# Kernel tuning notes

Measured on AMD Instinct MI355X. Metric: run time of the kernel, lower is better.

Reference implementation:

```python
import jax, jax.numpy as jnp
import numpy as np

N = 8192  # graph nodes (input_size)
B = 8     # batch size
MAX_DIFFUSION_STEP = 2
K_TOT = 2 * MAX_DIFFUSION_STEP + 1  # 2 kernels * 2 steps + identity term


def setup_inputs() -> dict:
    key = jax.random.key(0)
    k_in, k_h, k0, k1, k_w, k_b = jax.random.split(key, 6)
    scale = 0.5 / np.sqrt(N)  # keep spectral norm ~<1 so Chebyshev recursion is stable
    return {
        "input": jax.random.normal(k_in, (B, N), dtype=jnp.float32),
        "hidden": jax.random.normal(k_h, (B, N), dtype=jnp.float32),
        "kernel0": jax.random.normal(k0, (N, N), dtype=jnp.float32) * scale,
        "kernel1": jax.random.normal(k1, (N, N), dtype=jnp.float32) * scale,
        "W": jax.random.normal(k_w, (1, 2 * K_TOT), dtype=jnp.float32) * 0.1,
        "b": jax.random.normal(k_b, (1,), dtype=jnp.float32) * 0.1,
    }


def reference(input, hidden, kernel0, kernel1, W, b):
    batch_size, n = input.shape
    x0 = jnp.stack([input, hidden], axis=2)  # (B, N, 2)
    outs = [x0]
    for kernel in (kernel0, kernel1):
        x1 = jnp.einsum('ij,bjc->bic', kernel, x0)  # (B, N, 2)
        outs.append(x1)
        xp, xpp = x1, x0
        for _ in range(2, MAX_DIFFUSION_STEP + 1):
            x2 = 2.0 * jnp.einsum('ij,bjc->bic', kernel, xp) - xpp
            outs.append(x2)
            xp, xpp = x2, xp
    x = jnp.stack(outs, axis=0)  # (K_TOT, B, N, 2), row-major contiguous
    # Bug-compatible with torch .view: raw row-major reinterpretation
    x = x.reshape(K_TOT, n, 2, batch_size)
    x = jnp.transpose(x, (3, 1, 2, 0))          # (B, N, 2, K_TOT)
    x = x.reshape(batch_size * n, 2 * K_TOT)
    out = x @ W.T + b                           # Linear(2*K_TOT -> 1)
    return out.reshape(batch_size, n)
```

## Files before the change

kernel.cpp:

```cpp
#include <hip/hip_runtime.h>

#define N 8192
#define BATCH 8
#define CJ 256
#define NITER (N / CJ)

__global__ __launch_bounds__(256) void pack_x0_kernel(
    const float* __restrict__ input, const float* __restrict__ hidden,
    float* __restrict__ x0, float* __restrict__ x0t) {
  int j = blockIdx.x * 256 + threadIdx.x;
  #pragma unroll
  for (int b = 0; b < BATCH; ++b) {
    float vi = input[(size_t)b * N + j];
    float vh = hidden[(size_t)b * N + j];
    x0[(size_t)j * 16 + 2 * b]     = vi;
    x0[(size_t)j * 16 + 2 * b + 1] = vh;
    x0t[(size_t)(2 * b) * N + j]     = vi;
    x0t[(size_t)(2 * b + 1) * N + j] = vh;
  }
}

__global__ __launch_bounds__(256) void gemm16_kernel(
    const float* __restrict__ Km, const float* __restrict__ XT,
    const float* __restrict__ Xsub,
    float* __restrict__ Y, float* __restrict__ YT,
    float alpha, float beta) {
  __shared__ float Xs[2][16][CJ];
  __shared__ float red[256 * 33];
  const int wave = threadIdx.x >> 6;
  const int lane = threadIdx.x & 63;
  const int jl = lane * 4;
  const int i0 = blockIdx.x * 16 + wave * 4;

  float acc[4][16];
  #pragma unroll
  for (int r = 0; r < 4; ++r)
    #pragma unroll
    for (int c = 0; c < 16; ++c) acc[r][c] = 0.f;

  #pragma unroll
  for (int c2 = 0; c2 < 4; ++c2) {
    int c = c2 * 4 + wave;
    const float* gp = XT + (size_t)c * N + jl;
    __builtin_amdgcn_global_load_lds(
        (__attribute__((address_space(1))) void*)gp,
        (__attribute__((address_space(3))) void*)&Xs[0][c][0], 16, 0, 0);
  }
  float4 kfA[4], kfB[4];
  #pragma unroll
  for (int r = 0; r < 4; ++r)
    kfA[r] = *(const float4*)(Km + (size_t)(i0 + r) * N + jl);
  __syncthreads();

  int p = 0;
  for (int m = 0; m < NITER; ++m) {
    if (m + 1 < NITER) {
      int jn = (m + 1) * CJ + jl;
      #pragma unroll
      for (int c2 = 0; c2 < 4; ++c2) {
        int c = c2 * 4 + wave;
        const float* gp = XT + (size_t)c * N + jn;
        __builtin_amdgcn_global_load_lds(
            (__attribute__((address_space(1))) void*)gp,
            (__attribute__((address_space(3))) void*)&Xs[p ^ 1][c][0], 16, 0, 0);
      }
      #pragma unroll
      for (int r = 0; r < 4; ++r)
        kfB[r] = *(const float4*)(Km + (size_t)(i0 + r) * N + jn);
    }
    #pragma unroll
    for (int c = 0; c < 16; ++c) {
      float4 x = *(const float4*)&Xs[p][c][jl];
      #pragma unroll
      for (int r = 0; r < 4; ++r) {
        acc[r][c] = fmaf(kfA[r].x, x.x, acc[r][c]);
        acc[r][c] = fmaf(kfA[r].y, x.y, acc[r][c]);
        acc[r][c] = fmaf(kfA[r].z, x.z, acc[r][c]);
        acc[r][c] = fmaf(kfA[r].w, x.w, acc[r][c]);
      }
    }
    __syncthreads();
    if (m + 1 < NITER) {
      #pragma unroll
      for (int r = 0; r < 4; ++r) kfA[r] = kfB[r];
    }
    p ^= 1;
  }

  float total = 0.f;
  #pragma unroll
  for (int r = 0; r < 2; ++r)
    #pragma unroll
    for (int c = 0; c < 16; ++c)
      red[threadIdx.x * 33 + r * 16 + c] = acc[r][c];
  __syncthreads();
  if (lane < 32) {
    float s = 0.f;
    #pragma unroll
    for (int lp = 0; lp < 64; ++lp)
      s += red[(wave * 64 + lp) * 33 + lane];
    total = s;
  }
  __syncthreads();
  #pragma unroll
  for (int r = 0; r < 2; ++r)
    #pragma unroll
    for (int c = 0; c < 16; ++c)
      red[threadIdx.x * 33 + r * 16 + c] = acc[r + 2][c];
  __syncthreads();
  if (lane >= 32) {
    float s = 0.f;
    #pragma unroll
    for (int lp = 0; lp < 64; ++lp)
      s += red[(wave * 64 + lp) * 33 + (lane - 32)];
    total = s;
  }

  const int r = lane >> 4, c = lane & 15;
  const int row = i0 + r;
  float v = alpha * total;
  if (Xsub) v += beta * Xsub[(size_t)row * 16 + c];
  Y[(size_t)row * 16 + c] = v;
  if (YT) YT[(size_t)c * N + row] = v;
}

__global__ __launch_bounds__(256) void out_kernel(
    const float* __restrict__ X0, const float* __restrict__ X1a,
    const float* __restrict__ X2a, const float* __restrict__ X1b,
    const float* __restrict__ X2b, const float* __restrict__ W,
    const float* __restrict__ bias, float* __restrict__ out) {
  int tid = blockIdx.x * 256 + threadIdx.x;
  int b2 = tid >> 13;
  int i  = tid & (N - 1);
  int col = 2 * (i >> 10) + (b2 & 1);
  const float* Xs[5] = {X0, X1a, X2a, X1b, X2b};
  float accv = bias[0];
  #pragma unroll
  for (int c2 = 0; c2 < 2; ++c2) {
    int n = (i & 1023) * 8 + c2 * 4 + (b2 >> 1);
    #pragma unroll
    for (int k = 0; k < 5; ++k)
      accv += W[c2 * 5 + k] * Xs[k][(size_t)n * 16 + col];
  }
  out[tid] = accv;
}

extern "C" void kernel_launch(void* const* d_in, const int* in_sizes, int n_in,
                              void* d_out, int out_size, void* d_ws, size_t ws_size,
                              hipStream_t stream) {
  const float* input  = (const float*)d_in[0];
  const float* hidden = (const float*)d_in[1];
  const float* k0     = (const float*)d_in[2];
  const float* k1     = (const float*)d_in[3];
  const float* W      = (const float*)d_in[4];
  const float* bias   = (const float*)d_in[5];
  float* out = (float*)d_out;

  float* ws = (float*)d_ws;
  const size_t SZ = (size_t)N * 16;
  float* X0   = ws;
  float* X0T  = ws + SZ;
  float* X1a  = ws + 2 * SZ;
  float* X1aT = ws + 3 * SZ;
  float* X2a  = ws + 4 * SZ;
  float* X1b  = ws + 5 * SZ;
  float* X1bT = ws + 6 * SZ;
  float* X2b  = ws + 7 * SZ;

  pack_x0_kernel<<<N / 256, 256, 0, stream>>>(input, hidden, X0, X0T);
  gemm16_kernel<<<N / 16, 256, 0, stream>>>(k0, X0T,  nullptr, X1a, X1aT, 1.f, 0.f);
  gemm16_kernel<<<N / 16, 256, 0, stream>>>(k0, X1aT, X0,      X2a, nullptr, 2.f, -1.f);
  gemm16_kernel<<<N / 16, 256, 0, stream>>>(k1, X0T,  nullptr, X1b, X1bT, 1.f, 0.f);
  gemm16_kernel<<<N / 16, 256, 0, stream>>>(k1, X1bT, X0,      X2b, nullptr, 2.f, -1.f);

  out_kernel<<<(BATCH * N) / 256, 256, 0, stream>>>(X0, X1a, X2a, X1b, X2b, W, bias, out);
}
```

Baseline: 660.6 us.

## Batch both diffusion kernels into one GEMM launch per step and alias shared memory

Merges the kernel0 and kernel1 GEMMs for each Chebyshev step into a single launch of 1024 blocks, where the block index picks the matrix, input and output set. This cuts four GEMM launches to two and doubles the number of blocks per launch, which should fill the GPU better and hide tail effects. The shared-memory staging buffer and the reduction buffer now share one allocation, lowering LDS use per block, and launch bounds ask for 4 blocks per CU. The risk is extra register pressure from the occupancy hint and the need for the aliased reduction to stay safe after the final barrier.

```diff
diff --git a/kernel.cpp b/kernel.cpp
--- a/kernel.cpp
+++ b/kernel.cpp
@@ -20,17 +20,27 @@
   }
 }
 
-__global__ __launch_bounds__(256) void gemm16_kernel(
-    const float* __restrict__ Km, const float* __restrict__ XT,
+__global__ __launch_bounds__(256, 4) void gemm16x2_kernel(
+    const float* __restrict__ Km0, const float* __restrict__ Km1,
+    const float* __restrict__ XT0, const float* __restrict__ XT1,
     const float* __restrict__ Xsub,
-    float* __restrict__ Y, float* __restrict__ YT,
+    float* __restrict__ Y0, float* __restrict__ Y1,
+    float* __restrict__ YT0, float* __restrict__ YT1,
     float alpha, float beta) {
-  __shared__ float Xs[2][16][CJ];
-  __shared__ float red[256 * 33];
+  __shared__ float smem[256 * 33];
+  float (*Xs)[16][CJ] = (float (*)[16][CJ])smem;
+  float* red = smem;
+
   const int wave = threadIdx.x >> 6;
   const int lane = threadIdx.x & 63;
   const int jl = lane * 4;
-  const int i0 = blockIdx.x * 16 + wave * 4;
+  const int half = blockIdx.x >> 9;
+  const int blk  = blockIdx.x & 511;
+  const float* __restrict__ Km = half ? Km1 : Km0;
+  const float* __restrict__ XT = half ? XT1 : XT0;
+  float* Y  = half ? Y1 : Y0;
+  float* YT = half ? YT1 : YT0;
+  const int i0 = blk * 16 + wave * 4;
 
   float acc[4][16];
   #pragma unroll
@@ -168,10 +178,10 @@
   float* X2b  = ws + 7 * SZ;
 
   pack_x0_kernel<<<N / 256, 256, 0, stream>>>(input, hidden, X0, X0T);
-  gemm16_kernel<<<N / 16, 256, 0, stream>>>(k0, X0T,  nullptr, X1a, X1aT, 1.f, 0.f);
-  gemm16_kernel<<<N / 16, 256, 0, stream>>>(k0, X1aT, X0,      X2a, nullptr, 2.f, -1.f);
-  gemm16_kernel<<<N / 16, 256, 0, stream>>>(k1, X0T,  nullptr, X1b, X1bT, 1.f, 0.f);
-  gemm16_kernel<<<N / 16, 256, 0, stream>>>(k1, X1bT, X0,      X2b, nullptr, 2.f, -1.f);
-
-  out_kernel<<<(BATCH * N) / 256, 256, 0, stream>>>(X0, X1a, X2a, X1b, X2b, W, bias, out);
+  gemm16x2_kernel<<<2 * (N / 16), 256, 0, stream>>>(
+      k0, k1, X0T, X0T, nullptr, X1a, X1b, X1aT, X1bT, 1.f, 0.f);
+  gemm16x2_kernel<<<2 * (N / 16), 256, 0, stream>>>(
+      k0, k1, X1aT, X1bT, X0, X2a, X2b, nullptr, nullptr, 2.f, -1.f);
+  out_kernel<<<(BATCH * N) / 256, 256, 0, stream>>>(
+      X0, X1a, X2a, X1b, X2b, W, bias, out);
 }
```

Measured after the change: 701.8 us. 6.2% more time.

## Halve rows per block, deepen K prefetch, alias LDS for occupancy

Applied to the files above, without the earlier changes.

The GEMV-like kernel now gives each block 8 rows (2 per wave) instead of 16, doubling the grid to 1024 blocks. Kernel-matrix fragments are prefetched two chunks ahead through a 4-slot register ring. The per-iteration __syncthreads is replaced by a manual vmcnt wait plus s_barrier so the in-flight kernel loads stay outstanding. The reduction buffer aliases the X staging LDS and launch_bounds asks for 4 blocks per SM, aiming for more waves in flight to hide HBM latency on the bandwidth-bound matrix stream. The cost is that X is re-read from L2 by twice as many blocks, and the hand-tuned waitcnt depends on how the compiler orders memory operations.

```diff
diff --git a/kernel.cpp b/kernel.cpp
--- a/kernel.cpp
+++ b/kernel.cpp
@@ -4,6 +4,8 @@
 #define BATCH 8
 #define CJ 256
 #define NITER (N / CJ)
+#define ROWS 8
+#define RPW 2
 
 __global__ __launch_bounds__(256) void pack_x0_kernel(
     const float* __restrict__ input, const float* __restrict__ hidden,
@@ -20,23 +22,27 @@
   }
 }
 
-__global__ __launch_bounds__(256) void gemm16_kernel(
+__global__ __launch_bounds__(256, 4) void gemm8_kernel(
     const float* __restrict__ Km, const float* __restrict__ XT,
     const float* __restrict__ Xsub,
     float* __restrict__ Y, float* __restrict__ YT,
     float alpha, float beta) {
-  __shared__ float Xs[2][16][CJ];
-  __shared__ float red[256 * 33];
+  __shared__ float smem[256 * 33];
+  float (*Xs)[16][CJ] = (float (*)[16][CJ])smem;
+  float* red = smem;
+
   const int wave = threadIdx.x >> 6;
   const int lane = threadIdx.x & 63;
   const int jl = lane * 4;
-  const int i0 = blockIdx.x * 16 + wave * 4;
+  const int i0 = blockIdx.x * ROWS + wave * RPW;
 
-  float acc[4][16];
+  float acc[RPW][16];
   #pragma unroll
-  for (int r = 0; r < 4; ++r)
+  for (int r = 0; r < RPW; ++r)
     #pragma unroll
     for (int c = 0; c < 16; ++c) acc[r][c] = 0.f;
+
+  float4 kf[4][RPW];
 
   #pragma unroll
   for (int c2 = 0; c2 < 4; ++c2) {
@@ -46,50 +52,64 @@
         (__attribute__((address_space(1))) void*)gp,
         (__attribute__((address_space(3))) void*)&Xs[0][c][0], 16, 0, 0);
   }
-  float4 kfA[4], kfB[4];
+  asm volatile("" ::: "memory");
   #pragma unroll
-  for (int r = 0; r < 4; ++r)
-    kfA[r] = *(const float4*)(Km + (size_t)(i0 + r) * N + jl);
+  for (int r = 0; r < RPW; ++r) {
+    kf[0][r] = *(const float4*)(Km + (size_t)(i0 + r) * N + jl);
+    kf[1][r] = *(const float4*)(Km + (size_t)(i0 + r) * N + CJ + jl);
+  }
   __syncthreads();
 
-  int p = 0;
-  for (int m = 0; m < NITER; ++m) {
-    if (m + 1 < NITER) {
-      int jn = (m + 1) * CJ + jl;
-      #pragma unroll
-      for (int c2 = 0; c2 < 4; ++c2) {
-        int c = c2 * 4 + wave;
-        const float* gp = XT + (size_t)c * N + jn;
-        __builtin_amdgcn_global_load_lds(
-            (__attribute__((address_space(1))) void*)gp,
-            (__attribute__((address_space(3))) void*)&Xs[p ^ 1][c][0], 16, 0, 0);
+  for (int g = 0; g < NITER / 4; ++g) {
+    #pragma unroll
+    for (int mm = 0; mm < 4; ++mm) {
+      const int m = g * 4 + mm;
+      const int p = mm & 1;
+      if (m + 1 < NITER) {
+        int jn = (m + 1) * CJ + jl;
+        #pragma unroll
+        for (int c2 = 0; c2 < 4; ++c2) {
+          int c = c2 * 4 + wave;
+          const float* gp = XT + (size_t)c * N + jn;
+          __builtin_amdgcn_global_load_lds(
+              (__attribute__((address_space(1))) void*)gp,
+              (__attribute__((address_space(3))) void*)&Xs[p ^ 1][c][0],
+              16, 0, 0);
+        }
+      }
+      asm volatile("" ::: "memory");
+      if (m + 2 < NITER) {
+        int j2 = (m + 2) * CJ + jl;
+        #pragma unroll
+        for (int r = 0; r < RPW; ++r)
+          kf[(mm + 2) & 3][r] =
+              *(const float4*)(Km + (size_t)(i0 + r) * N + j2);
       }
       #pragma unroll
-      for (int r = 0; r < 4; ++r)
-        kfB[r] = *(const float4*)(Km + (size_t)(i0 + r) * N + jn);
-    }
-    #pragma unroll
-    for (int c = 0; c < 16; ++c) {
-      float4 x = *(const float4*)&Xs[p][c][jl];
-      #pragma unroll
-      for (int r = 0; r < 4; ++r) {
-        acc[r][c] = fmaf(kfA[r].x, x.x, acc[r][c]);
-        acc[r][c] = fmaf(kfA[r].y, x.y, acc[r][c]);
-        acc[r][c] = fmaf(kfA[r].z, x.z, acc[r][c]);
-        acc[r][c] = fmaf(kfA[r].w, x.w, acc[r][c]);
+      for (int c = 0; c < 16; ++c) {
+        float4 x = *(const float4*)&Xs[p][c][jl];
+        #pragma unroll
+        for (int r = 0; r < RPW; ++r) {
+          acc[r][c] = fmaf(kf[mm][r].x, x.x, acc[r][c]);
+          acc[r][c] = fmaf(kf[mm][r].y, x.y, acc[r][c]);
+          acc[r][c] = fmaf(kf[mm][r].z, x.z, acc[r][c]);
+          acc[r][c] = fmaf(kf[mm][r].w, x.w, acc[r][c]);
+        }
+      }
+      if (m + 1 < NITER) {
+        if (m + 2 < NITER)
+          asm volatile("s_waitcnt vmcnt(2)" ::: "memory");
+        else
+          asm volatile("s_waitcnt vmcnt(0)" ::: "memory");
+        __builtin_amdgcn_s_barrier();
+        __builtin_amdgcn_sched_barrier(0);
       }
     }
-    __syncthreads();
-    if (m + 1 < NITER) {
-      #pragma unroll
-      for (int r = 0; r < 4; ++r) kfA[r] = kfB[r];
-    }
-    p ^= 1;
   }
 
-  float total = 0.f;
+  __syncthreads();
   #pragma unroll
-  for (int r = 0; r < 2; ++r)
+  for (int r = 0; r < RPW; ++r)
     #pragma unroll
     for (int c = 0; c < 16; ++c)
       red[threadIdx.x * 33 + r * 16 + c] = acc[r][c];
@@ -99,29 +119,13 @@
     #pragma unroll
     for (int lp = 0; lp < 64; ++lp)
       s += red[(wave * 64 + lp) * 33 + lane];
-    total = s;
+    const int r = lane >> 4, c = lane & 15;
+    const int row = i0 + r;
+    float v = alpha * s;
+    if (Xsub) v += beta * Xsub[(size_t)row * 16 + c];
+    Y[(size_t)row * 16 + c] = v;
+    if (YT) YT[(size_t)c * N + row] = v;
   }
-  __syncthreads();
-  #pragma unroll
-  for (int r = 0; r < 2; ++r)
-    #pragma unroll
-    for (int c = 0; c < 16; ++c)
-      red[threadIdx.x * 33 + r * 16 + c] = acc[r + 2][c];
-  __syncthreads();
-  if (lane >= 32) {
-    float s = 0.f;
-    #pragma unroll
-    for (int lp = 0; lp < 64; ++lp)
-      s += red[(wave * 64 + lp) * 33 + (lane - 32)];
-    total = s;
-  }
-
-  const int r = lane >> 4, c = lane & 15;
-  const int row = i0 + r;
-  float v = alpha * total;
-  if (Xsub) v += beta * Xsub[(size_t)row * 16 + c];
-  Y[(size_t)row * 16 + c] = v;
-  if (YT) YT[(size_t)c * N + row] = v;
 }
 
 __global__ __launch_bounds__(256) void out_kernel(
@@ -168,10 +172,11 @@
   float* X2b  = ws + 7 * SZ;
 
   pack_x0_kernel<<<N / 256, 256, 0, stream>>>(input, hidden, X0, X0T);
-  gemm16_kernel<<<N / 16, 256, 0, stream>>>(k0, X0T,  nullptr, X1a, X1aT, 1.f, 0.f);
-  gemm16_kernel<<<N / 16, 256, 0, stream>>>(k0, X1aT, X0,      X2a, nullptr, 2.f, -1.f);
-  gemm16_kernel<<<N / 16, 256, 0, stream>>>(k1, X0T,  nullptr, X1b, X1bT, 1.f, 0.f);
-  gemm16_kernel<<<N / 16, 256, 0, stream>>>(k1, X1bT, X0,      X2b, nullptr, 2.f, -1.f);
+  gemm8_kernel<<<N / ROWS, 256, 0, stream>>>(k0, X0T,  nullptr, X1a, X1aT, 1.f, 0.f);
+  gemm8_kernel<<<N / ROWS, 256, 0, stream>>>(k0, X1aT, X0,      X2a, nullptr, 2.f, -1.f);
+  gemm8_kernel<<<N / ROWS, 256, 0, stream>>>(k1, X0T,  nullptr, X1b, X1bT, 1.f, 0.f);
+  gemm8_kernel<<<N / ROWS, 256, 0, stream>>>(k1, X1bT, X0,      X2b, nullptr, 2.f, -1.f);
 
-  out_kernel<<<(BATCH * N) / 256, 256, 0, stream>>>(X0, X1a, X2a, X1b, X2b, W, bias, out);
+  out_kernel<<<(BATCH * N) / 256, 256, 0, stream>>>(
+      X0, X1a, X2a, X1b, X2b, W, bias, out);
 }
```

Result: slower. 824.7 us (+24.8%).

## Split GEMV reduction dimension across two blocks and combine partials separately

Applied to the files above, without the earlier changes.

Each matrix pass now launches twice as many blocks, each reducing over half of the K dimension, and writes partial sums. A new combine kernel adds the partials and applies the alpha/beta Chebyshev update and transpose. Shared memory for the X tiles and the reduction buffer is aliased, and launch bounds request 4 blocks per CU to raise occupancy. The goal is better saturation of the CUs on the memory-bound 8192x8192 reads, at the cost of four extra small kernel launches and partial-buffer traffic.

```diff
diff --git a/kernel.cpp b/kernel.cpp
--- a/kernel.cpp
+++ b/kernel.cpp
@@ -3,7 +3,8 @@
 #define N 8192
 #define BATCH 8
 #define CJ 256
-#define NITER (N / CJ)
+#define JH 4096
+#define NITER_H (JH / CJ)
 
 __global__ __launch_bounds__(256) void pack_x0_kernel(
     const float* __restrict__ input, const float* __restrict__ hidden,
@@ -20,17 +21,21 @@
   }
 }
 
-__global__ __launch_bounds__(256) void gemm16_kernel(
+__global__ __launch_bounds__(256, 4) void gemm16s_kernel(
     const float* __restrict__ Km, const float* __restrict__ XT,
-    const float* __restrict__ Xsub,
-    float* __restrict__ Y, float* __restrict__ YT,
-    float alpha, float beta) {
-  __shared__ float Xs[2][16][CJ];
-  __shared__ float red[256 * 33];
+    float* __restrict__ Yp0, float* __restrict__ Yp1) {
+  __shared__ float smem[256 * 33];
+  float (*Xs)[16][CJ] = (float (*)[16][CJ])smem;
+  float* red = smem;
+
   const int wave = threadIdx.x >> 6;
   const int lane = threadIdx.x & 63;
   const int jl = lane * 4;
-  const int i0 = blockIdx.x * 16 + wave * 4;
+  const int h  = blockIdx.x & 1;
+  const int g  = blockIdx.x >> 1;
+  const int i0 = g * 16 + wave * 4;
+  const int j0 = h * JH;
+  float* __restrict__ Yp = h ? Yp1 : Yp0;
 
   float acc[4][16];
   #pragma unroll
@@ -41,7 +46,7 @@
   #pragma unroll
   for (int c2 = 0; c2 < 4; ++c2) {
     int c = c2 * 4 + wave;
-    const float* gp = XT + (size_t)c * N + jl;
+    const float* gp = XT + (size_t)c * N + j0 + jl;
     __builtin_amdgcn_global_load_lds(
         (__attribute__((address_space(1))) void*)gp,
         (__attribute__((address_space(3))) void*)&Xs[0][c][0], 16, 0, 0);
@@ -49,13 +54,13 @@
   float4 kfA[4], kfB[4];
   #pragma unroll
   for (int r = 0; r < 4; ++r)
-    kfA[r] = *(const float4*)(Km + (size_t)(i0 + r) * N + jl);
+    kfA[r] = *(const float4*)(Km + (size_t)(i0 + r) * N + j0 + jl);
   __syncthreads();
 
   int p = 0;
-  for (int m = 0; m < NITER; ++m) {
-    if (m + 1 < NITER) {
-      int jn = (m + 1) * CJ + jl;
+  for (int m = 0; m < NITER_H; ++m) {
+    if (m + 1 < NITER_H) {
+      int jn = j0 + (m + 1) * CJ + jl;
       #pragma unroll
       for (int c2 = 0; c2 < 4; ++c2) {
         int c = c2 * 4 + wave;
@@ -80,7 +85,7 @@
       }
     }
     __syncthreads();
-    if (m + 1 < NITER) {
+    if (m + 1 < NITER_H) {
       #pragma unroll
       for (int r = 0; r < 4; ++r) kfA[r] = kfB[r];
     }
@@ -118,10 +123,19 @@
 
   const int r = lane >> 4, c = lane & 15;
   const int row = i0 + r;
-  float v = alpha * total;
-  if (Xsub) v += beta * Xsub[(size_t)row * 16 + c];
-  Y[(size_t)row * 16 + c] = v;
-  if (YT) YT[(size_t)c * N + row] = v;
+  Yp[(size_t)row * 16 + c] = total;
+}
+
+__global__ __launch_bounds__(256) void combine_kernel(
+    const float* __restrict__ Yp0, const float* __restrict__ Yp1,
+    const float* __restrict__ Xsub,
+    float* __restrict__ Y, float* __restrict__ YT,
+    float alpha, float beta) {
+  int t = blockIdx.x * 256 + threadIdx.x;
+  float v = alpha * (Yp0[t] + Yp1[t]);
+  if (Xsub) v += beta * Xsub[t];
+  Y[t] = v;
+  if (YT) YT[(size_t)(t & 15) * N + (t >> 4)] = v;
 }
 
 __global__ __launch_bounds__(256) void out_kernel(
@@ -166,12 +180,22 @@
   float* X1b  = ws + 5 * SZ;
   float* X1bT = ws + 6 * SZ;
   float* X2b  = ws + 7 * SZ;
+  float* P0   = ws + 8 * SZ;
+  float* P1   = ws + 9 * SZ;
+
+  const int GB = 2 * (N / 16);
+  const int CB = (N * 16) / 256;
 
   pack_x0_kernel<<<N / 256, 256, 0, stream>>>(input, hidden, X0, X0T);
-  gemm16_kernel<<<N / 16, 256, 0, stream>>>(k0, X0T,  nullptr, X1a, X1aT, 1.f, 0.f);
-  gemm16_kernel<<<N / 16, 256, 0, stream>>>(k0, X1aT, X0,      X2a, nullptr, 2.f, -1.f);
-  gemm16_kernel<<<N / 16, 256, 0, stream>>>(k1, X0T,  nullptr, X1b, X1bT, 1.f, 0.f);
-  gemm16_kernel<<<N / 16, 256, 0, stream>>>(k1, X1bT, X0,      X2b, nullptr, 2.f, -1.f);
-
-  out_kernel<<<(BATCH * N) / 256, 256, 0, stream>>>(X0, X1a, X2a, X1b, X2b, W, bias, out);
-}
+  gemm16s_kernel<<<GB, 256, 0, stream>>>(k0, X0T, P0, P1);
+  combine_kernel<<<CB, 256, 0, stream>>>(P0, P1, nullptr, X1a, X1aT, 1.f, 0.f);
+  gemm16s_kernel<<<GB, 256, 0, stream>>>(k0, X1aT, P0, P1);
+  combine_kernel<<<CB, 256, 0, stream>>>(P0, P1, X0, X2a, nullptr, 2.f, -1.f);
+  gemm16s_kernel<<<GB, 256, 0, stream>>>(k1, X0T, P0, P1);
+  combine_kernel<<<CB, 256, 0, stream>>>(P0, P1, nullptr, X1b, X1bT, 1.f, 0.f);
+  gemm16s_kernel<<<GB, 256, 0, stream>>>(k1, X1bT, P0, P1);
+  combine_kernel<<<CB, 256, 0, stream>>>(P0, P1, X0, X2b, nullptr, 2.f, -1.f);
+
+  out_kernel<<<(BATCH * N) / 256, 256, 0, stream>>>(
+      X0, X1a, X2a, X1b, X2b, W, bias, out);
+}
```

Result: slower. 755.2 us (+14.3%).
